# Kernel tuning notes

Hardware: AMD Instinct MI355X
Metric: run time of the kernel (lower is better)

The kernel has to match this reference:

```python
import jax, jax.numpy as jnp
import numpy as np

N_NODES = 10000
N_EDGES = 160000
N_FEAT = 128      # n_features
N_BASIS = 20      # n_basis
N_LAYERS = 3      # n_interactions
N_GRAPHS = 64
CUTOFF = 5.0
VOCAB = 119       # 118 elements + padding idx 0


def setup_inputs() -> dict:
    key = jax.random.key(0)
    ks = jax.random.split(key, 20)
    z = jax.random.randint(ks[0], (N_NODES,), 0, VOCAB)
    pos = jax.random.normal(ks[1], (N_NODES, 3), dtype=jnp.float32) * 2.0
    cell = jax.random.normal(ks[2], (N_GRAPHS, 3, 3), dtype=jnp.float32)
    batch = jnp.sort(jax.random.randint(ks[3], (N_NODES,), 0, N_GRAPHS))
    edge_index = jax.random.randint(ks[4], (2, N_EDGES), 0, N_NODES)

    s = 1.0 / np.sqrt(N_FEAT)
    node_emb = jax.random.normal(ks[5], (VOCAB, N_FEAT), dtype=jnp.float32) * 0.1
    node_emb = node_emb.at[0].set(0.0)  # padding_idx=0
    # per-layer stacked parameters (L, ...)
    mnp_W1 = jax.random.normal(ks[6], (N_LAYERS, N_FEAT, N_FEAT), dtype=jnp.float32) * s
    mnp_b1 = jnp.zeros((N_LAYERS, N_FEAT), dtype=jnp.float32)
    mnp_W2 = jax.random.normal(ks[7], (N_LAYERS, N_FEAT, N_FEAT), dtype=jnp.float32) * s
    mnp_b2 = jnp.zeros((N_LAYERS, N_FEAT), dtype=jnp.float32)
    me_W = jax.random.normal(ks[8], (N_LAYERS, N_BASIS, N_FEAT), dtype=jnp.float32) * (1.0 / np.sqrt(N_BASIS))
    em1_W1 = jax.random.normal(ks[9], (N_LAYERS, N_FEAT, N_FEAT), dtype=jnp.float32) * s
    em1_W2 = jax.random.normal(ks[10], (N_LAYERS, N_FEAT, N_FEAT), dtype=jnp.float32) * s
    em2_W1 = jax.random.normal(ks[11], (N_LAYERS, N_FEAT, N_FEAT), dtype=jnp.float32) * s
    em2_W2 = jax.random.normal(ks[12], (N_LAYERS, N_FEAT, N_FEAT), dtype=jnp.float32) * s
    eu_W = jax.random.normal(ks[13], (N_LAYERS, N_FEAT, N_FEAT), dtype=jnp.float32) * s
    return {
        "z": z, "pos": pos, "cell": cell, "batch": batch, "edge_index": edge_index,
        "node_emb": node_emb,
        "mnp_W1": mnp_W1, "mnp_b1": mnp_b1, "mnp_W2": mnp_W2, "mnp_b2": mnp_b2,
        "me_W": me_W, "em1_W1": em1_W1, "em1_W2": em1_W2,
        "em2_W1": em2_W1, "em2_W2": em2_W2, "eu_W": eu_W,
    }


def _edge_embedding(pos_d, edge_index):
    """Gaussian RBF x cosine cutoff; dir = unit displacement vectors."""
    i, j = edge_index[0], edge_index[1]
    diff = pos_d[j] - pos_d[i]                      # (E, 3)
    d = jnp.sqrt(jnp.sum(diff * diff, axis=-1) + 1e-12)  # (E,)
    dir_edge = diff / d[:, None]                    # (E, 3)
    centers = jnp.linspace(0.0, CUTOFF, N_BASIS)
    width = CUTOFF / N_BASIS
    rbf = jnp.exp(-jnp.square((d[:, None] - centers) / width))  # (E, B)
    fc = 0.5 * (jnp.cos(jnp.pi * d / CUTOFF) + 1.0) * (d < CUTOFF)
    return rbf * fc[:, None], dir_edge


def reference(z, pos, cell, batch, edge_index, node_emb,
              mnp_W1, mnp_b1, mnp_W2, mnp_b2, me_W,
              em1_W1, em1_W2, em2_W1, em2_W2, eu_W):
    n = z.shape[0]
    atom = node_emb[z]                                   # (N, F)
    force = jnp.zeros((n, 3, N_FEAT), dtype=pos.dtype)   # (N, 3, F)

    # strain displacement bookkeeping (identity in plain forward)
    disp = jnp.broadcast_to(jnp.eye(3, dtype=pos.dtype), cell.shape)  # (G,3,3)
    sym = 0.5 * (disp + jnp.swapaxes(disp, -1, -2))
    pos_d = jnp.einsum('nd,nde->ne', pos, sym[batch])

    dist_edge, dir_edge = _edge_embedding(pos_d, edge_index)
    i, j = edge_index[0], edge_index[1]

    for l in range(N_LAYERS):
        # invariant node/edge message parts
        h = jax.nn.silu(atom @ mnp_W1[l] + mnp_b1[l]) @ mnp_W2[l] + mnp_b2[l]  # (N,F)
        me = dist_edge @ me_W[l]                                               # (E,F)
        msg = me * h[i] * h[j]                                                 # (E,F)
        atom = atom + jax.ops.segment_sum(msg, i, num_segments=n)
        # equivariant messages
        e1 = (jax.nn.silu(msg @ em1_W1[l]) @ em1_W2[l])[:, None, :] * dir_edge[:, :, None]  # (E,3,F)
        e2 = (jax.nn.silu(msg @ em2_W1[l]) @ em2_W2[l])[:, None, :] * force[j]              # (E,3,F)
        force = force + jax.ops.segment_sum(e1 + e2, i, num_segments=n)
        atom = atom + jnp.sum(force * (force @ eu_W[l]), axis=1)
    return atom, force
```

## Files before the change

### kernel.cpp

```cpp
#include <hip/hip_runtime.h>
#include <hip/hip_bf16.h>
#include <math.h>

#define NN 10000
#define NE 160000
#define NF 128
#define NB 20
#define CUT 5.0f
#define TPS 136
#define TPF 132

typedef __attribute__((ext_vector_type(8))) short short8;
typedef __attribute__((ext_vector_type(4))) float floatx4;
typedef unsigned short u16;
typedef unsigned int u32;

__device__ __forceinline__ u16 f2b(float x){
  union { __hip_bfloat16 b; u16 u; } cv;
  cv.b = __float2bfloat16(x);
  return cv.u;
}
__device__ __forceinline__ float lo_bf(u32 w){ return __uint_as_float(w << 16); }
__device__ __forceinline__ float hi_bf(u32 w){ return __uint_as_float(w & 0xFFFF0000u); }
__device__ __forceinline__ u32 packbf(float lo, float hi){
  return ((u32)f2b(hi) << 16) | (u32)f2b(lo);
}
__device__ __forceinline__ float fast_silu(float v){
  return v * __builtin_amdgcn_rcpf(1.f + __expf(-v));
}
__device__ __forceinline__ float rdf(const void* p, size_t i, int isb){
  return isb ? __bfloat162float(((const __hip_bfloat16*)p)[i]) : ((const float*)p)[i];
}

__global__ __launch_bounds__(256) void k_detect(const void* __restrict__ w, int nelem,
                                                int* __restrict__ flag){
  __shared__ int cnt;
  if (threadIdx.x == 0) cnt = 0;
  __syncthreads();
  const u16* hw = (const u16*)w;
  int local = 0;
  for (int k = threadIdx.x; k < nelem; k += 256){
    u16 h = hw[k];
    int e = (h >> 7) & 0xFF;
    if ((h & 0x7FFF) == 0 || (e >= 103 && e <= 130)) local++;
  }
  atomicAdd(&cnt, local);
  __syncthreads();
  if (threadIdx.x == 0) *flag = (cnt >= (nelem * 9) / 10) ? 1 : 0;
}

struct PrepArgs {
  const void* csrc[4]; float* cdst[4]; int cn[4];
  const void* ssrc[7]; u16* sdst[7];
  const void* mesrc;   u16* medst;
};
__global__ __launch_bounds__(256) void k_prep(PrepArgs a, const int* __restrict__ flag){
  int y = blockIdx.y;
  int isb = *flag;
  if (y < 4){
    const void* s = a.csrc[y]; float* d = a.cdst[y]; int n = a.cn[y];
    for (int i = blockIdx.x*256 + threadIdx.x; i < n; i += gridDim.x*256)
      d[i] = rdf(s, i, isb);
  } else if (y < 11){
    const void* s = a.ssrc[y-4]; u16* d = a.sdst[y-4];
    int idx = blockIdx.x*256 + threadIdx.x;
    int l = idx >> 14, rem = idx & 16383;
    int j = rem & 7, lane = (rem >> 3) & 63, tn = (rem >> 9) & 7, tk = rem >> 12;
    int k = tk*32 + ((lane >> 4) & 3)*8 + j, n = tn*16 + (lane & 15);
    d[idx] = f2b(rdf(s, (size_t)l*16384 + k*NF + n, isb));
  } else {
    int idx = blockIdx.x*256 + threadIdx.x;
    if (idx >= 3*4096) return;
    int l = idx >> 12, rem = idx & 4095;
    int j = rem & 7, lane = (rem >> 3) & 63, tn = rem >> 9;
    int k = ((lane >> 4) & 3)*8 + j, n = tn*16 + (lane & 15);
    a.medst[idx] = (k < NB) ? f2b(rdf(a.mesrc, (size_t)l*NB*NF + k*NF + n, isb)) : (u16)0;
  }
}

__global__ __launch_bounds__(256) void k_hist(const int* __restrict__ ei, int* __restrict__ count){
  int e = blockIdx.x*256 + threadIdx.x;
  if (e < NE) atomicAdd(&count[ei[e]], 1);
}
__global__ __launch_bounds__(256) void k_scan(const int* __restrict__ count,
                                              int* __restrict__ rowptr, int* __restrict__ cursor){
  __shared__ int part[256];
  const int CH = (NN + 255) / 256;
  int t = threadIdx.x;
  int base = t * CH;
  int s = 0;
  for (int k = 0; k < CH; k++){ int i = base + k; if (i < NN) s += count[i]; }
  part[t] = s;
  __syncthreads();
  for (int off = 1; off < 256; off <<= 1){
    int v = (t >= off) ? part[t - off] : 0;
    __syncthreads();
    part[t] += v;
    __syncthreads();
  }
  int run = (t == 0) ? 0 : part[t - 1];
  for (int k = 0; k < CH; k++){
    int i = base + k;
    if (i < NN){ rowptr[i] = run; cursor[i] = run; run += count[i]; }
  }
  if (t == 255) rowptr[NN] = run;
}
__global__ __launch_bounds__(256) void k_scatter_embed(const int* __restrict__ ei,
                                                       int* __restrict__ cursor,
                                                       const float* __restrict__ pos,
                                                       int* __restrict__ iis, int* __restrict__ jjs,
                                                       float* __restrict__ ds, float* __restrict__ dirs){
  int e = blockIdx.x * 256 + threadIdx.x;
  if (e >= NE) return;
  int i = ei[e], j = ei[NE + e];
  float dx = pos[j*3+0] - pos[i*3+0];
  float dy = pos[j*3+1] - pos[i*3+1];
  float dz = pos[j*3+2] - pos[i*3+2];
  float d = sqrtf(dx*dx + dy*dy + dz*dz + 1e-12f);
  float inv = 1.0f / d;
  int s = atomicAdd(&cursor[i], 1);
  iis[s] = i; jjs[s] = j;
  ds[s] = d;
  dirs[s*3+0] = dx*inv; dirs[s*3+1] = dy*inv; dirs[s*3+2] = dz*inv;
}

__global__ __launch_bounds__(64, 4) void k_mlp0(
    const int* __restrict__ z, const float* __restrict__ emb,
    float* __restrict__ atom,
    const u16* __restrict__ w1sw, const float* __restrict__ b1,
    const u16* __restrict__ w2sw, const float* __restrict__ b2,
    u32* __restrict__ hb)
{
  __shared__ __align__(16) u16 tileT[16][TPS];
  const int lane = threadIdx.x;
  const int q = lane >> 4, ln = lane & 15;
  const int n0 = blockIdx.x * 16;
  const int zn = z[n0 + ln];

  floatx4 c1[8];
  #pragma unroll
  for (int tn = 0; tn < 8; tn++) c1[tn] = (floatx4){0,0,0,0};
  #pragma unroll
  for (int tk = 0; tk < 4; tk++){
    const float4 u0 = *(const float4*)&emb[(size_t)zn*NF + tk*32 + q*8];
    const float4 u1 = *(const float4*)&emb[(size_t)zn*NF + tk*32 + q*8 + 4];
    *(float4*)&atom[(size_t)(n0+ln)*NF + tk*32 + q*8]     = u0;
    *(float4*)&atom[(size_t)(n0+ln)*NF + tk*32 + q*8 + 4] = u1;
    short8 a;
    a[0]=(short)f2b(u0.x); a[1]=(short)f2b(u0.y); a[2]=(short)f2b(u0.z); a[3]=(short)f2b(u0.w);
    a[4]=(short)f2b(u1.x); a[5]=(short)f2b(u1.y); a[6]=(short)f2b(u1.z); a[7]=(short)f2b(u1.w);
    #pragma unroll
    for (int tn = 0; tn < 8; tn++){
      short8 b = *(const short8*)(w1sw + (size_t)((tk*8 + tn)*64 + lane)*8);
      c1[tn] = __builtin_amdgcn_mfma_f32_16x16x32_bf16(a, b, c1[tn], 0, 0, 0);
    }
  }
  #pragma unroll
  for (int tn = 0; tn < 8; tn++){
    int n = tn*16 + ln;
    float bias = b1[n];
    #pragma unroll
    for (int r = 0; r < 4; r++)
      tileT[q*4 + r][n] = f2b(fast_silu(c1[tn][r] + bias));
  }
  floatx4 c2[8];
  #pragma unroll
  for (int tn = 0; tn < 8; tn++) c2[tn] = (floatx4){0,0,0,0};
  #pragma unroll
  for (int tk = 0; tk < 4; tk++){
    short8 a = *(const short8*)&tileT[ln][tk*32 + q*8];
    #pragma unroll
    for (int tn = 0; tn < 8; tn++){
      short8 b = *(const short8*)(w2sw + (size_t)((tk*8 + tn)*64 + lane)*8);
      c2[tn] = __builtin_amdgcn_mfma_f32_16x16x32_bf16(a, b, c2[tn], 0, 0, 0);
    }
  }
  float b2n[8];
  #pragma unroll
  for (int tn = 0; tn < 8; tn++) b2n[tn] = b2[tn*16 + ln];
  #pragma unroll
  for (int tn = 0; tn < 4; tn++){
    #pragma unroll
    for (int r = 0; r < 4; r++){
      float vl = c2[tn][r]   + b2n[tn];
      float vh = c2[tn+4][r] + b2n[tn+4];
      hb[(size_t)(n0 + q*4 + r)*64 + tn*16 + ln] = packbf(vl, vh);
    }
  }
}

#define SEGFLUSH(ADDR_EXPR)                                               \
  {                                                                       \
    float s_ = 0.f;                                                       \
    _Pragma("unroll")                                                     \
    for (int m_ = 0; m_ < 16; m_++){                                      \
      s_ += tileF[m_][cc];                                                \
      if (m_ == 15 || ((bmask >> (m_ + 1)) & 1u)){                        \
        int ii_ = __builtin_amdgcn_readlane(curii, m_);                   \
        float* p_ = (ADDR_EXPR);                                          \
        atomicAdd(p_ + cc, s_);                                           \
        s_ = 0.f;                                                         \
      }                                                                   \
    }                                                                     \
  }

__global__ __launch_bounds__(128, 4) void k_edge_mfma(
    const int* __restrict__ iis, const int* __restrict__ jjs,
    const float* __restrict__ ds, const float* __restrict__ dirs,
    const u32* __restrict__ hb,
    const u16* __restrict__ mesw,
    const u16* __restrict__ w11sw, const u16* __restrict__ w12sw,
    const u16* __restrict__ w21sw, const u16* __restrict__ w22sw,
    float* __restrict__ atom, const u32* __restrict__ forceb, float* __restrict__ fdelta)
{
  __shared__ __align__(16) u16 tileM[16][TPS];
  __shared__ __align__(16) float tileF[16][TPF];
  u16* tileFu = (u16*)&tileF[0][0];

  const int wv = threadIdx.x >> 6;
  const int lane = threadIdx.x & 63;
  const int q = lane >> 4, ln = lane & 15;
  const int bid = (blockIdx.x & 7) * (gridDim.x >> 3) + (blockIdx.x >> 3);
  const int e0 = bid * 16;
  const int cc = wv*64 + lane;

  const int l16 = lane & 15;
  int curii = iis[e0 + l16];
  int previi = (l16 == 0) ? ~curii : iis[e0 + l16 - 1];
  const u32 bmask = (u32)__ballot(lane < 16 && (curii != previi));

  int iiR[4], jjR[4];
  float dirR[4][3];
  #pragma unroll
  for (int r = 0; r < 4; r++){
    int s = e0 + q*4 + r;
    iiR[r] = iis[s]; jjR[r] = jjs[s];
    dirR[r][0] = dirs[s*3+0]; dirR[r][1] = dirs[s*3+1]; dirR[r][2] = dirs[s*3+2];
  }

  u32 hiw[4][4], hjw[4][4];
  #pragma unroll
  for (int r = 0; r < 4; r++)
    #pragma unroll
    for (int t = 0; t < 4; t++){
      hiw[r][t] = hb[(size_t)iiR[r]*64 + t*16 + ln];
      hjw[r][t] = hb[(size_t)jjR[r]*64 + t*16 + ln];
    }

  float dA  = ds[e0 + ln];
  float fcA = (dA < CUT) ? 0.5f*(cosf((float)M_PI*dA*(1.0f/CUT)) + 1.0f) : 0.0f;
  short8 a_rbf;
  #pragma unroll
  for (int j = 0; j < 8; j++){
    int k = q*8 + j;
    float v = 0.f;
    if (k < NB){
      float t = (dA - CUT*(float)k/(float)(NB-1)) * ((float)NB/CUT);
      v = __expf(-t*t) * fcA;
    }
    a_rbf[j] = (short)f2b(v);
  }

  #pragma unroll
  for (int t = 0; t < 4; t++){
    const int tn_g = wv*4 + t;
    short8 b = *(const short8*)(mesw + (size_t)(tn_g*64 + lane)*8);
    floatx4 c = {0.f,0.f,0.f,0.f};
    c = __builtin_amdgcn_mfma_f32_16x16x32_bf16(a_rbf, b, c, 0, 0, 0);
    const int n = tn_g*16 + ln;
    #pragma unroll
    for (int r = 0; r < 4; r++){
      float hi_ = wv ? hi_bf(hiw[r][t]) : lo_bf(hiw[r][t]);
      float hj_ = wv ? hi_bf(hjw[r][t]) : lo_bf(hjw[r][t]);
      float mv = c[r] * hi_ * hj_;
      tileF[q*4 + r][n] = mv;
      tileM[q*4 + r][n] = f2b(mv);
    }
  }

  SEGFLUSH(&atom[(size_t)ii_ * NF])

  __syncthreads();

  floatx4 c2[4], c1[4];
  #pragma unroll
  for (int t = 0; t < 4; t++){ c2[t] = (floatx4){0,0,0,0}; c1[t] = (floatx4){0,0,0,0}; }
  #pragma unroll
  for (int tk = 0; tk < 4; tk++){
    short8 a = *(const short8*)&tileM[ln][tk*32 + q*8];
    #pragma unroll
    for (int t = 0; t < 4; t++){
      const int tn_g = wv*4 + t;
      short8 b2 = *(const short8*)(w21sw + (size_t)((tk*8 + tn_g)*64 + lane)*8);
      c2[t] = __builtin_amdgcn_mfma_f32_16x16x32_bf16(a, b2, c2[t], 0, 0, 0);
      short8 b1 = *(const short8*)(w11sw + (size_t)((tk*8 + tn_g)*64 + lane)*8);
      c1[t] = __builtin_amdgcn_mfma_f32_16x16x32_bf16(a, b1, c1[t], 0, 0, 0);
    }
  }
  #pragma unroll
  for (int t = 0; t < 4; t++){
    const int n = (wv*4 + t)*16 + ln;
    #pragma unroll
    for (int r = 0; r < 4; r++){
      tileFu[(q*4 + r)*TPS + n] = f2b(fast_silu(c1[t][r]));
      c2[t][r] = fast_silu(c2[t][r]);
    }
  }

  __syncthreads();

  floatx4 g1[4];
  #pragma unroll
  for (int t = 0; t < 4; t++) g1[t] = (floatx4){0,0,0,0};
  #pragma unroll
  for (int tk = 0; tk < 4; tk++){
    short8 a = *(const short8*)&tileFu[(size_t)ln*TPS + tk*32 + q*8];
    #pragma unroll
    for (int t = 0; t < 4; t++){
      short8 b = *(const short8*)(w12sw + (size_t)((tk*8 + wv*4 + t)*64 + lane)*8);
      g1[t] = __builtin_amdgcn_mfma_f32_16x16x32_bf16(a, b, g1[t], 0, 0, 0);
    }
  }
  #pragma unroll
  for (int t = 0; t < 4; t++){
    const int n = (wv*4 + t)*16 + ln;
    #pragma unroll
    for (int r = 0; r < 4; r++) tileM[q*4 + r][n] = f2b(c2[t][r]);
  }

  __syncthreads();

  floatx4 g2[4];
  #pragma unroll
  for (int t = 0; t < 4; t++) g2[t] = (floatx4){0,0,0,0};
  #pragma unroll
  for (int tk = 0; tk < 4; tk++){
    short8 a = *(const short8*)&tileM[ln][tk*32 + q*8];
    #pragma unroll
    for (int t = 0; t < 4; t++){
      short8 b = *(const short8*)(w22sw + (size_t)((tk*8 + wv*4 + t)*64 + lane)*8);
      g2[t] = __builtin_amdgcn_mfma_f32_16x16x32_bf16(a, b, g2[t], 0, 0, 0);
    }
  }

  for (int d = 0; d < 3; d++){
    u32 fjw[4][4];
    #pragma unroll
    for (int r = 0; r < 4; r++)
      #pragma unroll
      for (int t = 0; t < 4; t++)
        fjw[r][t] = forceb[((size_t)jjR[r]*3 + d)*64 + t*16 + ln];
    #pragma unroll
    for (int t = 0; t < 4; t++){
      const int n = (wv*4 + t)*16 + ln;
      #pragma unroll
      for (int r = 0; r < 4; r++){
        float fj = wv ? hi_bf(fjw[r][t]) : lo_bf(fjw[r][t]);
        tileF[q*4 + r][n] = g1[t][r]*dirR[r][d] + g2[t][r]*fj;
      }
    }
    SEGFLUSH(&fdelta[((size_t)ii_*3 + d)*NF])
  }
}

__global__ __launch_bounds__(64, 2) void k_node(
    float* __restrict__ force, float* __restrict__ fdelta,
    const u16* __restrict__ eusw, u32* __restrict__ forceb,
    float* __restrict__ atom,
    const u16* __restrict__ w1sw, const float* __restrict__ b1,
    const u16* __restrict__ w2sw, const float* __restrict__ b2,
    u32* __restrict__ hb, int do_mlp)
{
  __shared__ __align__(16) u16 tile[16][TPS];
  __shared__ __align__(16) float tileF[16][TPF];
  const int lane = threadIdx.x;
  const int q = lane >> 4, ln = lane & 15;
  const int n0 = blockIdx.x * 16;

  float acc[8][4];
  #pragma unroll
  for (int tn = 0; tn < 8; tn++)
    #pragma unroll
    for (int r = 0; r < 4; r++) acc[tn][r] = 0.f;

  for (int d = 0; d < 3; d++){
    #pragma unroll
    for (int m = 0; m < 16; m++){
      size_t idx = ((size_t)(n0+m)*3 + d)*NF + lane;
      float v0 = force[idx]    + fdelta[idx];
      float v1 = force[idx+64] + fdelta[idx+64];
      force[idx] = v0; force[idx+64] = v1;
      fdelta[idx] = 0.f; fdelta[idx+64] = 0.f;
      forceb[((size_t)(n0+m)*3 + d)*64 + lane] = packbf(v0, v1);
      tile[m][lane]    = f2b(v0);
      tile[m][lane+64] = f2b(v1);
      tileF[m][lane]    = v0;
      tileF[m][lane+64] = v1;
    }
    floatx4 c[8];
    #pragma unroll
    for (int tn = 0; tn < 8; tn++) c[tn] = (floatx4){0,0,0,0};
    #pragma unroll
    for (int tk = 0; tk < 4; tk++){
      short8 a = *(const short8*)&tile[ln][tk*32 + q*8];
      #pragma unroll
      for (int tn = 0; tn < 8; tn++){
        short8 b = *(const short8*)(eusw + (size_t)((tk*8 + tn)*64 + lane)*8);
        c[tn] = __builtin_amdgcn_mfma_f32_16x16x32_bf16(a, b, c[tn], 0, 0, 0);
      }
    }
    #pragma unroll
    for (int tn = 0; tn < 8; tn++){
      int n = tn*16 + ln;
      #pragma unroll
      for (int r = 0; r < 4; r++)
        acc[tn][r] += tileF[q*4 + r][n] * c[tn][r];
    }
  }

  float anew[8][4];
  #pragma unroll
  for (int tn = 0; tn < 8; tn++){
    int n = tn*16 + ln;
    #pragma unroll
    for (int r = 0; r < 4; r++){
      size_t idx = (size_t)(n0 + q*4 + r)*NF + n;
      float v = atom[idx] + acc[tn][r];
      atom[idx] = v;
      anew[tn][r] = v;
    }
  }
  if (!do_mlp) return;

  #pragma unroll
  for (int tn = 0; tn < 8; tn++){
    int n = tn*16 + ln;
    #pragma unroll
    for (int r = 0; r < 4; r++) tile[q*4 + r][n] = f2b(anew[tn][r]);
  }
  floatx4 c1[8];
  #pragma unroll
  for (int tn = 0; tn < 8; tn++) c1[tn] = (floatx4){0,0,0,0};
  #pragma unroll
  for (int tk = 0; tk < 4; tk++){
    short8 a = *(const short8*)&tile[ln][tk*32 + q*8];
    #pragma unroll
    for (int tn = 0; tn < 8; tn++){
      short8 b = *(const short8*)(w1sw + (size_t)((tk*8 + tn)*64 + lane)*8);
      c1[tn] = __builtin_amdgcn_mfma_f32_16x16x32_bf16(a, b, c1[tn], 0, 0, 0);
    }
  }
  #pragma unroll
  for (int tn = 0; tn < 8; tn++){
    int n = tn*16 + ln;
    float bias = b1[n];
    #pragma unroll
    for (int r = 0; r < 4; r++)
      tile[q*4 + r][n] = f2b(fast_silu(c1[tn][r] + bias));
  }
  floatx4 c2[8];
  #pragma unroll
  for (int tn = 0; tn < 8; tn++) c2[tn] = (floatx4){0,0,0,0};
  #pragma unroll
  for (int tk = 0; tk < 4; tk++){
    short8 a = *(const short8*)&tile[ln][tk*32 + q*8];
    #pragma unroll
    for (int tn = 0; tn < 8; tn++){
      short8 b = *(const short8*)(w2sw + (size_t)((tk*8 + tn)*64 + lane)*8);
      c2[tn] = __builtin_amdgcn_mfma_f32_16x16x32_bf16(a, b, c2[tn], 0, 0, 0);
    }
  }
  float b2n[8];
  #pragma unroll
  for (int tn = 0; tn < 8; tn++) b2n[tn] = b2[tn*16 + ln];
  #pragma unroll
  for (int tn = 0; tn < 4; tn++){
    #pragma unroll
    for (int r = 0; r < 4; r++){
      float vl = c2[tn][r]   + b2n[tn];
      float vh = c2[tn+4][r] + b2n[tn+4];
      hb[(size_t)(n0 + q*4 + r)*64 + tn*16 + ln] = packbf(vl, vh);
    }
  }
}

__global__ __launch_bounds__(256) void k_writeout(const float* __restrict__ atom,
                                                  const float* __restrict__ force,
                                                  void* __restrict__ out,
                                                  const int* __restrict__ flag){
  int idx = blockIdx.x * 256 + threadIdx.x;
  const int na = NN * NF;
  const int tot = na + NN * 3 * NF;
  if (idx >= tot) return;
  float v = (idx < na) ? atom[idx] : force[idx - na];
  if (*flag) ((__hip_bfloat16*)out)[idx] = __float2bfloat16(v);
  else       ((float*)out)[idx] = v;
}

extern "C" void kernel_launch(void* const* d_in, const int* in_sizes, int n_in,
                              void* d_out, int out_size, void* d_ws, size_t ws_size,
                              hipStream_t stream){
  const int* z    = (const int*)d_in[0];
  const void* pos = d_in[1];
  const int* ei   = (const int*)d_in[4];
  const void* emb   = d_in[5];
  const void* mnpW1 = d_in[6];
  const void* mnpb1 = d_in[7];
  const void* mnpW2 = d_in[8];
  const void* mnpb2 = d_in[9];
  const void* meW   = d_in[10];
  const void* em1W1 = d_in[11];
  const void* em1W2 = d_in[12];
  const void* em2W1 = d_in[13];
  const void* em2W2 = d_in[14];
  const void* euW   = d_in[15];

  float* base  = (float*)d_ws;
  int*   flag  = (int*)d_ws;
  float* atom   = base + 4;
  float* force  = atom   + NN*NF;
  float* fdelta = force  + (size_t)NN*3*NF;
  u32*   forceb = (u32*)(fdelta + (size_t)NN*3*NF);
  int*   count  = (int*)(forceb + (size_t)NN*3*64);
  float* ds    = (float*)(count + NN);
  float* dirs  = ds + NE;
  float* posf  = dirs + 3*NE;
  float* embf  = posf + NN*3;
  float* b1f   = embf + 119*NF;
  float* b2f_  = b1f + 3*NF;
  u32*   hb    = (u32*)(b2f_ + 3*NF);
  u16*   mesw  = (u16*)(hb + (size_t)NN*64);
  u16*   w11sw = mesw  + 3*4096;
  u16*   w12sw = w11sw + 3*16384;
  u16*   w21sw = w12sw + 3*16384;
  u16*   w22sw = w21sw + 3*16384;
  u16*   w1sw  = w22sw + 3*16384;
  u16*   w2sw  = w1sw  + 3*16384;
  u16*   eusw  = w2sw  + 3*16384;
  int* rowptr  = (int*)(eusw + 3*16384);
  int* cursor  = rowptr + NN + 1;
  int* iis     = cursor + NN;
  int* jjs     = iis + NE;

  k_detect<<<1, 256, 0, stream>>>(meW, 3*NB*NF, flag);

  hipMemsetAsync(force, 0, ((size_t)NN*3*NF*2 + (size_t)NN*3*64 + NN)*4, stream);

  PrepArgs pa;
  pa.csrc[0]=pos;   pa.cdst[0]=posf; pa.cn[0]=NN*3;
  pa.csrc[1]=emb;   pa.cdst[1]=embf; pa.cn[1]=119*NF;
  pa.csrc[2]=mnpb1; pa.cdst[2]=b1f;  pa.cn[2]=3*NF;
  pa.csrc[3]=mnpb2; pa.cdst[3]=b2f_; pa.cn[3]=3*NF;
  pa.ssrc[0]=em1W1; pa.sdst[0]=w11sw;
  pa.ssrc[1]=em1W2; pa.sdst[1]=w12sw;
  pa.ssrc[2]=em2W1; pa.sdst[2]=w21sw;
  pa.ssrc[3]=em2W2; pa.sdst[3]=w22sw;
  pa.ssrc[4]=mnpW1; pa.sdst[4]=w1sw;
  pa.ssrc[5]=mnpW2; pa.sdst[5]=w2sw;
  pa.ssrc[6]=euW;   pa.sdst[6]=eusw;
  pa.mesrc=meW;     pa.medst=mesw;
  k_prep<<<dim3(192,12), 256, 0, stream>>>(pa, flag);

  k_hist         <<<(NE+255)/256, 256, 0, stream>>>(ei, count);
  k_scan         <<<1, 256, 0, stream>>>(count, rowptr, cursor);
  k_scatter_embed<<<(NE+255)/256, 256, 0, stream>>>(ei, cursor, posf, iis, jjs, ds, dirs);

  k_mlp0<<<NN/16, 64, 0, stream>>>(z, embf, atom, w1sw, b1f, w2sw, b2f_, hb);
  for (int l = 0; l < 3; l++){
    k_edge_mfma<<<NE/16, 128, 0, stream>>>(iis, jjs, ds, dirs, hb,
        mesw  + (size_t)l*4096,
        w11sw + (size_t)l*16384, w12sw + (size_t)l*16384,
        w21sw + (size_t)l*16384, w22sw + (size_t)l*16384,
        atom, forceb, fdelta);
    int nl = l + 1;
    k_node<<<NN/16, 64, 0, stream>>>(force, fdelta,
        eusw + (size_t)l*16384, forceb, atom,
        w1sw + (size_t)(nl%3)*16384, b1f + (size_t)(nl%3)*NF,
        w2sw + (size_t)(nl%3)*16384, b2f_ + (size_t)(nl%3)*NF,
        hb, (l < 2) ? 1 : 0);
  }

  k_writeout<<<(NN*NF + NN*3*NF + 255)/256, 256, 0, stream>>>(atom, force, d_out, flag);
}
```

Before: 561.1 us.

## Split node MLP and force-update kernels across two waves per block

k_mlp0 and k_node now launch 128 threads (two wavefronts) per 16-node block instead of one. Each wave computes half of the 128 output columns, and the shared-memory tiles are synchronized with __syncthreads. Bf16 outputs are written as 16-bit halves into the packed hb/forceb layout. The aim is to halve per-wave MFMA and register work and raise parallelism on these small node kernels, at the cost of extra barriers and narrower 16-bit stores.

After: 539.1 us. -3.9%, faster.

```diff
diff --git a/kernel.cpp b/kernel.cpp
--- a/kernel.cpp
+++ b/kernel.cpp
@@ -124,7 +124,7 @@
   dirs[s*3+0] = dx*inv; dirs[s*3+1] = dy*inv; dirs[s*3+2] = dz*inv;
 }
 
-__global__ __launch_bounds__(64, 4) void k_mlp0(
+__global__ __launch_bounds__(128, 2) void k_mlp0(
     const int* __restrict__ z, const float* __restrict__ emb,
     float* __restrict__ atom,
     const u16* __restrict__ w1sw, const float* __restrict__ b1,
@@ -132,60 +132,59 @@
     u32* __restrict__ hb)
 {
   __shared__ __align__(16) u16 tileT[16][TPS];
-  const int lane = threadIdx.x;
+  const int wv = threadIdx.x >> 6;
+  const int lane = threadIdx.x & 63;
   const int q = lane >> 4, ln = lane & 15;
   const int n0 = blockIdx.x * 16;
   const int zn = z[n0 + ln];
 
-  floatx4 c1[8];
-  #pragma unroll
-  for (int tn = 0; tn < 8; tn++) c1[tn] = (floatx4){0,0,0,0};
+  floatx4 c1[4];
+  #pragma unroll
+  for (int t = 0; t < 4; t++) c1[t] = (floatx4){0,0,0,0};
   #pragma unroll
   for (int tk = 0; tk < 4; tk++){
     const float4 u0 = *(const float4*)&emb[(size_t)zn*NF + tk*32 + q*8];
     const float4 u1 = *(const float4*)&emb[(size_t)zn*NF + tk*32 + q*8 + 4];
-    *(float4*)&atom[(size_t)(n0+ln)*NF + tk*32 + q*8]     = u0;
-    *(float4*)&atom[(size_t)(n0+ln)*NF + tk*32 + q*8 + 4] = u1;
+    if ((tk >> 1) == wv){
+      *(float4*)&atom[(size_t)(n0+ln)*NF + tk*32 + q*8]     = u0;
+      *(float4*)&atom[(size_t)(n0+ln)*NF + tk*32 + q*8 + 4] = u1;
+    }
     short8 a;
     a[0]=(short)f2b(u0.x); a[1]=(short)f2b(u0.y); a[2]=(short)f2b(u0.z); a[3]=(short)f2b(u0.w);
     a[4]=(short)f2b(u1.x); a[5]=(short)f2b(u1.y); a[6]=(short)f2b(u1.z); a[7]=(short)f2b(u1.w);
     #pragma unroll
-    for (int tn = 0; tn < 8; tn++){
-      short8 b = *(const short8*)(w1sw + (size_t)((tk*8 + tn)*64 + lane)*8);
-      c1[tn] = __builtin_amdgcn_mfma_f32_16x16x32_bf16(a, b, c1[tn], 0, 0, 0);
-    }
-  }
-  #pragma unroll
-  for (int tn = 0; tn < 8; tn++){
-    int n = tn*16 + ln;
+    for (int t = 0; t < 4; t++){
+      short8 b = *(const short8*)(w1sw + (size_t)((tk*8 + wv*4 + t)*64 + lane)*8);
+      c1[t] = __builtin_amdgcn_mfma_f32_16x16x32_bf16(a, b, c1[t], 0, 0, 0);
+    }
+  }
+  #pragma unroll
+  for (int t = 0; t < 4; t++){
+    int n = (wv*4 + t)*16 + ln;
     float bias = b1[n];
     #pragma unroll
     for (int r = 0; r < 4; r++)
-      tileT[q*4 + r][n] = f2b(fast_silu(c1[tn][r] + bias));
-  }
-  floatx4 c2[8];
-  #pragma unroll
-  for (int tn = 0; tn < 8; tn++) c2[tn] = (floatx4){0,0,0,0};
+      tileT[q*4 + r][n] = f2b(fast_silu(c1[t][r] + bias));
+  }
+  __syncthreads();
+  floatx4 c2[4];
+  #pragma unroll
+  for (int t = 0; t < 4; t++) c2[t] = (floatx4){0,0,0,0};
   #pragma unroll
   for (int tk = 0; tk < 4; tk++){
     short8 a = *(const short8*)&tileT[ln][tk*32 + q*8];
     #pragma unroll
-    for (int tn = 0; tn < 8; tn++){
-      short8 b = *(const short8*)(w2sw + (size_t)((tk*8 + tn)*64 + lane)*8);
-      c2[tn] = __builtin_amdgcn_mfma_f32_16x16x32_bf16(a, b, c2[tn], 0, 0, 0);
-    }
-  }
-  float b2n[8];
-  #pragma unroll
-  for (int tn = 0; tn < 8; tn++) b2n[tn] = b2[tn*16 + ln];
-  #pragma unroll
-  for (int tn = 0; tn < 4; tn++){
-    #pragma unroll
-    for (int r = 0; r < 4; r++){
-      float vl = c2[tn][r]   + b2n[tn];
-      float vh = c2[tn+4][r] + b2n[tn+4];
-      hb[(size_t)(n0 + q*4 + r)*64 + tn*16 + ln] = packbf(vl, vh);
-    }
+    for (int t = 0; t < 4; t++){
+      short8 b = *(const short8*)(w2sw + (size_t)((tk*8 + wv*4 + t)*64 + lane)*8);
+      c2[t] = __builtin_amdgcn_mfma_f32_16x16x32_bf16(a, b, c2[t], 0, 0, 0);
+    }
+  }
+  #pragma unroll
+  for (int t = 0; t < 4; t++){
+    float bias = b2[(wv*4 + t)*16 + ln];
+    #pragma unroll
+    for (int r = 0; r < 4; r++)
+      ((u16*)hb)[(((size_t)(n0 + q*4 + r))*64 + t*16 + ln)*2 + wv] = f2b(c2[t][r] + bias);
   }
 }
 
@@ -363,7 +362,7 @@
   }
 }
 
-__global__ __launch_bounds__(64, 2) void k_node(
+__global__ __launch_bounds__(128, 2) void k_node(
     float* __restrict__ force, float* __restrict__ fdelta,
     const u16* __restrict__ eusw, u32* __restrict__ forceb,
     float* __restrict__ atom,
@@ -371,116 +370,114 @@
     const u16* __restrict__ w2sw, const float* __restrict__ b2,
     u32* __restrict__ hb, int do_mlp)
 {
-  __shared__ __align__(16) u16 tile[16][TPS];
+  __shared__ __align__(16) u16 tileM[16][TPS];
   __shared__ __align__(16) float tileF[16][TPF];
-  const int lane = threadIdx.x;
+  const int wv = threadIdx.x >> 6;
+  const int lane = threadIdx.x & 63;
   const int q = lane >> 4, ln = lane & 15;
   const int n0 = blockIdx.x * 16;
-
-  float acc[8][4];
-  #pragma unroll
-  for (int tn = 0; tn < 8; tn++)
-    #pragma unroll
-    for (int r = 0; r < 4; r++) acc[tn][r] = 0.f;
+  const int cc = wv*64 + lane;
+
+  float acc[4][4];
+  #pragma unroll
+  for (int t = 0; t < 4; t++)
+    #pragma unroll
+    for (int r = 0; r < 4; r++) acc[t][r] = 0.f;
 
   for (int d = 0; d < 3; d++){
     #pragma unroll
     for (int m = 0; m < 16; m++){
-      size_t idx = ((size_t)(n0+m)*3 + d)*NF + lane;
-      float v0 = force[idx]    + fdelta[idx];
-      float v1 = force[idx+64] + fdelta[idx+64];
-      force[idx] = v0; force[idx+64] = v1;
-      fdelta[idx] = 0.f; fdelta[idx+64] = 0.f;
-      forceb[((size_t)(n0+m)*3 + d)*64 + lane] = packbf(v0, v1);
-      tile[m][lane]    = f2b(v0);
-      tile[m][lane+64] = f2b(v1);
-      tileF[m][lane]    = v0;
-      tileF[m][lane+64] = v1;
-    }
-    floatx4 c[8];
-    #pragma unroll
-    for (int tn = 0; tn < 8; tn++) c[tn] = (floatx4){0,0,0,0};
+      size_t idx = ((size_t)(n0+m)*3 + d)*NF + cc;
+      float v = force[idx] + fdelta[idx];
+      force[idx] = v; fdelta[idx] = 0.f;
+      ((u16*)forceb)[(((size_t)(n0+m)*3 + d)*64 + lane)*2 + wv] = f2b(v);
+      tileM[m][cc] = f2b(v);
+      tileF[m][cc] = v;
+    }
+    __syncthreads();
+    floatx4 c[4];
+    #pragma unroll
+    for (int t = 0; t < 4; t++) c[t] = (floatx4){0,0,0,0};
     #pragma unroll
     for (int tk = 0; tk < 4; tk++){
-      short8 a = *(const short8*)&tile[ln][tk*32 + q*8];
+      short8 a = *(const short8*)&tileM[ln][tk*32 + q*8];
       #pragma unroll
-      for (int tn = 0; tn < 8; tn++){
-        short8 b = *(const short8*)(eusw + (size_t)((tk*8 + tn)*64 + lane)*8);
-        c[tn] = __builtin_amdgcn_mfma_f32_16x16x32_bf16(a, b, c[tn], 0, 0, 0);
+      for (int t = 0; t < 4; t++){
+        short8 b = *(const short8*)(eusw + (size_t)((tk*8 + wv*4 + t)*64 + lane)*8);
+        c[t] = __builtin_amdgcn_mfma_f32_16x16x32_bf16(a, b, c[t], 0, 0, 0);
       }
     }
     #pragma unroll
-    for (int tn = 0; tn < 8; tn++){
-      int n = tn*16 + ln;
+    for (int t = 0; t < 4; t++){
+      int n = (wv*4 + t)*16 + ln;
       #pragma unroll
       for (int r = 0; r < 4; r++)
-        acc[tn][r] += tileF[q*4 + r][n] * c[tn][r];
-    }
-  }
-
-  float anew[8][4];
-  #pragma unroll
-  for (int tn = 0; tn < 8; tn++){
-    int n = tn*16 + ln;
+        acc[t][r] += tileF[q*4 + r][n] * c[t][r];
+    }
+    __syncthreads();
+  }
+
+  float anew[4][4];
+  #pragma unroll
+  for (int t = 0; t < 4; t++){
+    int n = (wv*4 + t)*16 + ln;
     #pragma unroll
     for (int r = 0; r < 4; r++){
       size_t idx = (size_t)(n0 + q*4 + r)*NF + n;
-      float v = atom[idx] + acc[tn][r];
+      float v = atom[idx] + acc[t][r];
       atom[idx] = v;
-      anew[tn][r] = v;
+      anew[t][r] = v;
     }
   }
   if (!do_mlp) return;
 
   #pragma unroll
-  for (int tn = 0; tn < 8; tn++){
-    int n = tn*16 + ln;
-    #pragma unroll
-    for (int r = 0; r < 4; r++) tile[q*4 + r][n] = f2b(anew[tn][r]);
-  }
-  floatx4 c1[8];
-  #pragma unroll
-  for (int tn = 0; tn < 8; tn++) c1[tn] = (floatx4){0,0,0,0};
-  #pragma unroll
-  for (int tk = 0; tk < 4; tk++){
-    short8 a = *(const short8*)&tile[ln][tk*32 + q*8];
-    #pragma unroll
-    for (int tn = 0; tn < 8; tn++){
-      short8 b = *(const short8*)(w1sw + (size_t)((tk*8 + tn)*64 + lane)*8);
-      c1[tn] = __builtin_amdgcn_mfma_f32_16x16x32_bf16(a, b, c1[tn], 0, 0, 0);
-    }
-  }
-  #pragma unroll
-  for (int tn = 0; tn < 8; tn++){
-    int n = tn*16 + ln;
+  for (int t = 0; t < 4; t++){
+    int n = (wv*4 + t)*16 + ln;
+    #pragma unroll
+    for (int r = 0; r < 4; r++) tileM[q*4 + r][n] = f2b(anew[t][r]);
+  }
+  __syncthreads();
+  floatx4 c1[4];
+  #pragma unroll
+  for (int t = 0; t < 4; t++) c1[t] = (floatx4){0,0,0,0};
+  #pragma unroll
+  for (int tk = 0; tk < 4; tk++){
+    short8 a = *(const short8*)&tileM[ln][tk*32 + q*8];
+    #pragma unroll
+    for (int t = 0; t < 4; t++){
+      short8 b = *(const short8*)(w1sw + (size_t)((tk*8 + wv*4 + t)*64 + lane)*8);
+      c1[t] = __builtin_amdgcn_mfma_f32_16x16x32_bf16(a, b, c1[t], 0, 0, 0);
+    }
+  }
+  __syncthreads();
+  #pragma unroll
+  for (int t = 0; t < 4; t++){
+    int n = (wv*4 + t)*16 + ln;
     float bias = b1[n];
     #pragma unroll
     for (int r = 0; r < 4; r++)
-      tile[q*4 + r][n] = f2b(fast_silu(c1[tn][r] + bias));
-  }
-  floatx4 c2[8];
-  #pragma unroll
-  for (int tn = 0; tn < 8; tn++) c2[tn] = (floatx4){0,0,0,0};
-  #pragma unroll
-  for (int tk = 0; tk < 4; tk++){
-    short8 a = *(const short8*)&tile[ln][tk*32 + q*8];
-    #pragma unroll
-    for (int tn = 0; tn < 8; tn++){
-      short8 b = *(const short8*)(w2sw + (size_t)((tk*8 + tn)*64 + lane)*8);
-      c2[tn] = __builtin_amdgcn_mfma_f32_16x16x32_bf16(a, b, c2[tn], 0, 0, 0);
-    }
-  }
-  float b2n[8];
-  #pragma unroll
-  for (int tn = 0; tn < 8; tn++) b2n[tn] = b2[tn*16 + ln];
-  #pragma unroll
-  for (int tn = 0; tn < 4; tn++){
-    #pragma unroll
-    for (int r = 0; r < 4; r++){
-      float vl = c2[tn][r]   + b2n[tn];
-      float vh = c2[tn+4][r] + b2n[tn+4];
-      hb[(size_t)(n0 + q*4 + r)*64 + tn*16 + ln] = packbf(vl, vh);
-    }
+      tileM[q*4 + r][n] = f2b(fast_silu(c1[t][r] + bias));
+  }
+  __syncthreads();
+  floatx4 c2[4];
+  #pragma unroll
+  for (int t = 0; t < 4; t++) c2[t] = (floatx4){0,0,0,0};
+  #pragma unroll
+  for (int tk = 0; tk < 4; tk++){
+    short8 a = *(const short8*)&tileM[ln][tk*32 + q*8];
+    #pragma unroll
+    for (int t = 0; t < 4; t++){
+      short8 b = *(const short8*)(w2sw + (size_t)((tk*8 + wv*4 + t)*64 + lane)*8);
+      c2[t] = __builtin_amdgcn_mfma_f32_16x16x32_bf16(a, b, c2[t], 0, 0, 0);
+    }
+  }
+  #pragma unroll
+  for (int t = 0; t < 4; t++){
+    float bias = b2[(wv*4 + t)*16 + ln];
+    #pragma unroll
+    for (int r = 0; r < 4; r++)
+      ((u16*)hb)[(((size_t)(n0 + q*4 + r))*64 + t*16 + ln)*2 + wv] = f2b(c2[t][r] + bias);
   }
 }
 
@@ -565,7 +562,7 @@
   k_scan         <<<1, 256, 0, stream>>>(count, rowptr, cursor);
   k_scatter_embed<<<(NE+255)/256, 256, 0, stream>>>(ei, cursor, posf, iis, jjs, ds, dirs);
 
-  k_mlp0<<<NN/16, 64, 0, stream>>>(z, embf, atom, w1sw, b1f, w2sw, b2f_, hb);
+  k_mlp0<<<NN/16, 128, 0, stream>>>(z, embf, atom, w1sw, b1f, w2sw, b2f_, hb);
   for (int l = 0; l < 3; l++){
     k_edge_mfma<<<NE/16, 128, 0, stream>>>(iis, jjs, ds, dirs, hb,
         mesw  + (size_t)l*4096,
@@ -573,7 +570,7 @@
         w21sw + (size_t)l*16384, w22sw + (size_t)l*16384,
         atom, forceb, fdelta);
     int nl = l + 1;
-    k_node<<<NN/16, 64, 0, stream>>>(force, fdelta,
+    k_node<<<NN/16, 128, 0, stream>>>(force, fdelta,
         eusw + (size_t)l*16384, forceb, atom,
         w1sw + (size_t)(nl%3)*16384, b1f + (size_t)(nl%3)*NF,
         w2sw + (size_t)(nl%3)*16384, b2f_ + (size_t)(nl%3)*NF,
```
